# Optimization experiments

Measured on AMD Instinct MI355X. Metric: run time of the kernel, lower is better.

## Reference

```python
import jax, jax.numpy as jnp
import numpy as np

BN_EPS = 1e-5


def setup_inputs() -> dict:
    key = jax.random.key(0)
    ks = jax.random.split(key, 8)
    B, T, D, Tu, Dout, M = 32, 4096, 128, 512, 64, 8
    feats = jax.random.normal(ks[0], (B, T, D), dtype=jnp.float32)
    # integer time-window ids stored in channel 0 of x; pin 0 and Tu-1 so
    # tw_uniq = arange(0, Tu) exactly (no -99 padding) for every batch row
    tw = jax.random.randint(ks[1], (B, T), 0, Tu)
    tw = tw.at[:, 0].set(0).at[:, 1].set(Tu - 1)
    x = jnp.concatenate([tw[..., None].astype(jnp.float32), feats], axis=-1)
    mask = jax.random.uniform(ks[2], (B, T, 1)) < 0.9
    mask = mask.at[:, :2].set(True)  # keep pinned min/max entries valid
    tw_uniq = jnp.broadcast_to(jnp.arange(Tu, dtype=jnp.float32)[None, :, None], (B, Tu, 1))
    bn_gamma = jax.random.uniform(ks[3], (D,), jnp.float32, 0.5, 1.5)
    bn_beta = 0.1 * jax.random.normal(ks[4], (D,), dtype=jnp.float32)
    bn_mean = jnp.zeros((D,), jnp.float32)
    bn_var = jnp.ones((D,), jnp.float32)
    conv_w = jax.random.normal(ks[5], (Dout, D), dtype=jnp.float32) / np.float32(np.sqrt(D))
    conv_b = jnp.zeros((Dout,), jnp.float32)
    fc_w = jax.random.normal(ks[6], (M, Dout), dtype=jnp.float32) / np.float32(np.sqrt(Dout))
    fc_b = jnp.zeros((M,), jnp.float32)
    return dict(x=x, mask=mask, tw_uniq=tw_uniq, bn_gamma=bn_gamma, bn_beta=bn_beta,
                bn_mean=bn_mean, bn_var=bn_var, conv_w=conv_w, conv_b=conv_b,
                fc_w=fc_w, fc_b=fc_b)


def reference(x, mask, tw_uniq, bn_gamma, bn_beta, bn_mean, bn_var,
              conv_w, conv_b, fc_w, fc_b):
    # --- TimeWindowPooling (segment-max form of the dense expand+where+amax) ---
    # torch computes amax_T(where(tw==tw_uniq & mask, x, 0)) -> max(0, group max).
    # Equivalent: scatter-max of mask-zeroed values into a zeros-initialized
    # (B, Tu, D) buffer, avoiding the O(B*T*Tu*D) blowup.
    tw = x[..., 0]           # (B, T) integer-valued, detached in torch
    feats = x[..., 1:]       # (B, T, D)
    B, T, D = feats.shape
    Tu = tw_uniq.shape[1]
    u0 = tw_uniq[:, 0, 0]    # per-batch window minimum
    idx = jnp.clip((tw - u0[:, None]).astype(jnp.int32), 0, Tu - 1)  # (B, T)
    vals = jnp.where(mask, feats, 0.0)  # masked rows contribute 0 == init value
    hidden = jnp.zeros((B, Tu, D), feats.dtype).at[jnp.arange(B)[:, None], idx].max(vals)
    # --- mlp_down: BatchNorm1d (inference stats) + 1x1 Conv1d over channels ---
    h = (hidden - bn_mean) * jax.lax.rsqrt(bn_var + BN_EPS) * bn_gamma + bn_beta
    h = jnp.einsum('bud,od->buo', h, conv_w) + conv_b  # (B, Tu, Dout)
    # --- fc_out ---
    return jnp.einsum('buo,mo->bum', h, fc_w) + fc_b   # (B, Tu, M)
```

## Files before the change

### kernel.cpp

```cpp
#include <hip/hip_runtime.h>

#define B_   32
#define T_   4096
#define D_   128
#define TU   512
#define M_   8
#define O_   64
#define BN_EPS 1e-5f

typedef float f4u __attribute__((ext_vector_type(4), aligned(4)));

#define WS_UIDX   0
#define WS_BASE   (B_ * T_)
#define WS_END    (WS_BASE + B_ * TU)
#define WS_ROWIDX (WS_END + B_ * TU)


__global__ __launch_bounds__(256) void index_kernel(
    const float* __restrict__ x, const int* __restrict__ mask,
    const float* __restrict__ tw_uniq, int* __restrict__ wsI) {
    const int g = blockIdx.x * 256 + threadIdx.x;
    const int b = g >> 12;
    const float twf = x[(size_t)g * (D_ + 1)];
    const int   mk  = mask[g];
    const float u0  = tw_uniq[b * TU];
    const int   u   = min(max((int)(twf - u0), 0), TU - 1);
    wsI[WS_UIDX + g] = mk ? u : -1;
}

__global__ __launch_bounds__(1024) void build_kernel(int* __restrict__ wsI) {
    __shared__ int cnt[TU];
    __shared__ int scn[TU];
    __shared__ int cur[TU];
    const int b = blockIdx.x;
    const int tid = threadIdx.x;
    if (tid < TU) cnt[tid] = 0;
    __syncthreads();
    const int* ub = wsI + WS_UIDX + b * T_;
    int uv[4];
#pragma unroll
    for (int r = 0; r < 4; ++r) {
        uv[r] = ub[r * 1024 + tid];
        if (uv[r] >= 0) atomicAdd(&cnt[uv[r]], 1);
    }
    __syncthreads();
    if (tid < TU) scn[tid] = cnt[tid];
    __syncthreads();
    for (int off = 1; off < TU; off <<= 1) {
        int v = 0;
        if (tid < TU && tid >= off) v = scn[tid - off];
        __syncthreads();
        if (tid < TU) scn[tid] += v;
        __syncthreads();
    }
    if (tid < TU) {
        const int e = scn[tid];
        const int s = e - cnt[tid];
        wsI[WS_BASE + b * TU + tid] = s;
        wsI[WS_END  + b * TU + tid] = e;
        cur[tid] = s;
    }
    __syncthreads();
    int* rb = wsI + WS_ROWIDX + b * T_;
#pragma unroll
    for (int r = 0; r < 4; ++r) {
        if (uv[r] >= 0) {
            const int pos = atomicAdd(&cur[uv[r]], 1);
            rb[pos] = r * 1024 + tid;
        }
    }
}

__global__ __launch_bounds__(1024) void gather_mm_kernel(
    const float* __restrict__ x,
    const float* __restrict__ bn_gamma, const float* __restrict__ bn_beta,
    const float* __restrict__ bn_mean,  const float* __restrict__ bn_var,
    const float* __restrict__ conv_w,   const float* __restrict__ conv_b,
    const float* __restrict__ fc_w,     const float* __restrict__ fc_b,
    const int* __restrict__ wsI, float* __restrict__ out) {
    __shared__ float wsm[M_ * D_];
    __shared__ float tmp[M_ * D_];
    __shared__ float biasc[M_];
    const int j = blockIdx.x;
    const int b  = (j & 7) + 8 * ((j >> 3) & 3);
    const int uc = j >> 5;
    const int tid = threadIdx.x;

    {
        const int m = tid >> 7, d = tid & (D_ - 1);
        float wraw = 0.f;
        for (int o = 0; o < O_; ++o) wraw += fc_w[m * O_ + o] * conv_w[o * D_ + d];
        const float sc = bn_gamma[d] * rsqrtf(bn_var[d] + BN_EPS);
        const float sh = bn_beta[d] - bn_mean[d] * sc;
        wsm[tid] = wraw * sc;
        tmp[tid] = wraw * sh;
    }
    __syncthreads();
    if (tid < M_) {
        float s = fc_b[tid];
        for (int o = 0; o < O_; ++o) s += fc_w[tid * O_ + o] * conv_b[o];
        for (int d = 0; d < D_; ++d) s += tmp[tid * D_ + d];
        biasc[tid] = s;
    }
    __syncthreads();

    const int w    = tid >> 6;
    const int lane = tid & 63;
    const int half = lane >> 5;
    const int lq   = lane & 31;
    const float* xb = x + (size_t)b * T_ * (D_ + 1);
    const int* rowb = wsI + WS_ROWIDX + b * T_;

    for (int k = 0; k < 4; ++k) {
        const int u = uc * 64 + w * 4 + k;
        const int start = wsI[WS_BASE + b * TU + u];
        const int end   = wsI[WS_END  + b * TU + u];
        float a0 = 0.f, a1 = 0.f, a2 = 0.f, a3 = 0.f;
        int  r    = start + half;
        bool have = r < end;
        f4u  vn;
        if (have) { vn = *(const f4u*)(xb + (size_t)rowb[r] * (D_ + 1) + 1 + lq * 4); r += 2; }
        while (have) {
            const f4u v = vn;
            have = r < end;
            if (have) { vn = *(const f4u*)(xb + (size_t)rowb[r] * (D_ + 1) + 1 + lq * 4); r += 2; }
            a0 = fmaxf(a0, v.x); a1 = fmaxf(a1, v.y);
            a2 = fmaxf(a2, v.z); a3 = fmaxf(a3, v.w);
        }
        a0 = fmaxf(a0, __shfl_xor(a0, 32)); a1 = fmaxf(a1, __shfl_xor(a1, 32));
        a2 = fmaxf(a2, __shfl_xor(a2, 32)); a3 = fmaxf(a3, __shfl_xor(a3, 32));

        const int db = lq * 4;
        float p0, p1, p2, p3, p4, p5, p6, p7;
#define PDOT(mm) (a0 * wsm[(mm) * D_ + db] + a1 * wsm[(mm) * D_ + db + 1] + \
                  a2 * wsm[(mm) * D_ + db + 2] + a3 * wsm[(mm) * D_ + db + 3])
        p0 = PDOT(0); p1 = PDOT(1); p2 = PDOT(2); p3 = PDOT(3);
        p4 = PDOT(4); p5 = PDOT(5); p6 = PDOT(6); p7 = PDOT(7);
#undef PDOT
#pragma unroll
        for (int off = 1; off < 32; off <<= 1) {
            p0 += __shfl_xor(p0, off); p1 += __shfl_xor(p1, off);
            p2 += __shfl_xor(p2, off); p3 += __shfl_xor(p3, off);
            p4 += __shfl_xor(p4, off); p5 += __shfl_xor(p5, off);
            p6 += __shfl_xor(p6, off); p7 += __shfl_xor(p7, off);
        }
        if (lane == 0) {
            float* op = out + ((size_t)(b * TU + u)) * M_;
            *(float4*)(op)     = make_float4(p0 + biasc[0], p1 + biasc[1],
                                             p2 + biasc[2], p3 + biasc[3]);
            *(float4*)(op + 4) = make_float4(p4 + biasc[4], p5 + biasc[5],
                                             p6 + biasc[6], p7 + biasc[7]);
        }
    }
}

extern "C" void kernel_launch(void* const* d_in, const int* in_sizes, int n_in,
                              void* d_out, int out_size, void* d_ws, size_t ws_size,
                              hipStream_t stream) {
    const float* x        = (const float*)d_in[0];
    const int*   mask     = (const int*)  d_in[1];
    const float* tw_uniq  = (const float*)d_in[2];
    const float* bn_gamma = (const float*)d_in[3];
    const float* bn_beta  = (const float*)d_in[4];
    const float* bn_mean  = (const float*)d_in[5];
    const float* bn_var   = (const float*)d_in[6];
    const float* conv_w   = (const float*)d_in[7];
    const float* conv_b   = (const float*)d_in[8];
    const float* fc_w     = (const float*)d_in[9];
    const float* fc_b     = (const float*)d_in[10];
    int*   wsI = (int*)d_ws;
    float* out = (float*)d_out;

    index_kernel<<<512, 256, 0, stream>>>(x, mask, tw_uniq, wsI);
    build_kernel<<<32, 1024, 0, stream>>>(wsI);
    gather_mm_kernel<<<256, 1024, 0, stream>>>(
        x, bn_gamma, bn_beta, bn_mean, bn_var,
        conv_w, conv_b, fc_w, fc_b, wsI, out);
}
```

Before: 141.6 us.

## Fuse index pass into build kernel and give each half-wave its own window

The separate index kernel is folded into the per-batch build kernel, which computes window ids straight from x and mask and keeps them in shared memory. The gather kernel now assigns one window per half-wavefront rather than four windows per wavefront. It doubles the grid and batches up to 8 row loads at a time, using row indices broadcast by shuffle, to raise memory-level parallelism. This removes one launch and a global round trip, but only 32 blocks now read the strided x timestamps, and the extra gather blocks repeat the weight-folding prologue.

```diff
diff --git a/kernel.cpp b/kernel.cpp
--- a/kernel.cpp
+++ b/kernel.cpp
@@ -10,25 +10,15 @@
 
 typedef float f4u __attribute__((ext_vector_type(4), aligned(4)));
 
-#define WS_UIDX   0
-#define WS_BASE   (B_ * T_)
-#define WS_END    (WS_BASE + B_ * TU)
-#define WS_ROWIDX (WS_END + B_ * TU)
+#define WS_BASE   0
+#define WS_END    (B_ * TU)
+#define WS_ROWIDX (2 * B_ * TU)
 
 
-__global__ __launch_bounds__(256) void index_kernel(
+__global__ __launch_bounds__(1024) void build_kernel(
     const float* __restrict__ x, const int* __restrict__ mask,
     const float* __restrict__ tw_uniq, int* __restrict__ wsI) {
-    const int g = blockIdx.x * 256 + threadIdx.x;
-    const int b = g >> 12;
-    const float twf = x[(size_t)g * (D_ + 1)];
-    const int   mk  = mask[g];
-    const float u0  = tw_uniq[b * TU];
-    const int   u   = min(max((int)(twf - u0), 0), TU - 1);
-    wsI[WS_UIDX + g] = mk ? u : -1;
-}
-
-__global__ __launch_bounds__(1024) void build_kernel(int* __restrict__ wsI) {
+    __shared__ int uloc[T_];
     __shared__ int cnt[TU];
     __shared__ int scn[TU];
     __shared__ int cur[TU];
@@ -36,12 +26,17 @@
     const int tid = threadIdx.x;
     if (tid < TU) cnt[tid] = 0;
     __syncthreads();
-    const int* ub = wsI + WS_UIDX + b * T_;
-    int uv[4];
+    const float* xb = x + (size_t)b * T_ * (D_ + 1);
+    const int*   mb = mask + b * T_;
+    const float  u0 = tw_uniq[b * TU];
 #pragma unroll
     for (int r = 0; r < 4; ++r) {
-        uv[r] = ub[r * 1024 + tid];
-        if (uv[r] >= 0) atomicAdd(&cnt[uv[r]], 1);
+        const int t = r * 1024 + tid;
+        const float twf = xb[(size_t)t * (D_ + 1)];
+        const int   mk  = mb[t];
+        const int   u   = min(max((int)(twf - u0), 0), TU - 1);
+        uloc[t] = mk ? u : -1;
+        if (mk) atomicAdd(&cnt[u], 1);
     }
     __syncthreads();
     if (tid < TU) scn[tid] = cnt[tid];
@@ -64,14 +59,16 @@
     int* rb = wsI + WS_ROWIDX + b * T_;
 #pragma unroll
     for (int r = 0; r < 4; ++r) {
-        if (uv[r] >= 0) {
-            const int pos = atomicAdd(&cur[uv[r]], 1);
-            rb[pos] = r * 1024 + tid;
+        const int t = r * 1024 + tid;
+        const int u = uloc[t];
+        if (u >= 0) {
+            const int pos = atomicAdd(&cur[u], 1);
+            rb[pos] = t;
         }
     }
 }
 
-__global__ __launch_bounds__(1024) void gather_mm_kernel(
+__global__ __launch_bounds__(1024, 4) void gather_mm_kernel(
     const float* __restrict__ x,
     const float* __restrict__ bn_gamma, const float* __restrict__ bn_beta,
     const float* __restrict__ bn_mean,  const float* __restrict__ bn_var,
@@ -111,46 +108,63 @@
     const float* xb = x + (size_t)b * T_ * (D_ + 1);
     const int* rowb = wsI + WS_ROWIDX + b * T_;
 
-    for (int k = 0; k < 4; ++k) {
-        const int u = uc * 64 + w * 4 + k;
-        const int start = wsI[WS_BASE + b * TU + u];
-        const int end   = wsI[WS_END  + b * TU + u];
-        float a0 = 0.f, a1 = 0.f, a2 = 0.f, a3 = 0.f;
-        int  r    = start + half;
-        bool have = r < end;
-        f4u  vn;
-        if (have) { vn = *(const f4u*)(xb + (size_t)rowb[r] * (D_ + 1) + 1 + lq * 4); r += 2; }
-        while (have) {
-            const f4u v = vn;
-            have = r < end;
-            if (have) { vn = *(const f4u*)(xb + (size_t)rowb[r] * (D_ + 1) + 1 + lq * 4); r += 2; }
-            a0 = fmaxf(a0, v.x); a1 = fmaxf(a1, v.y);
-            a2 = fmaxf(a2, v.z); a3 = fmaxf(a3, v.w);
-        }
-        a0 = fmaxf(a0, __shfl_xor(a0, 32)); a1 = fmaxf(a1, __shfl_xor(a1, 32));
-        a2 = fmaxf(a2, __shfl_xor(a2, 32)); a3 = fmaxf(a3, __shfl_xor(a3, 32));
+    const int u     = uc * 32 + w * 2 + half;
+    const int start = wsI[WS_BASE + b * TU + u];
+    const int end   = wsI[WS_END  + b * TU + u];
+    const int n     = end - start;
+    const int nn    = min(n, 32);
+    int myidx = 0;
+    if (lq < n) myidx = rowb[start + lq];
 
-        const int db = lq * 4;
-        float p0, p1, p2, p3, p4, p5, p6, p7;
+    float a0 = 0.f, a1 = 0.f, a2 = 0.f, a3 = 0.f;
+#define ROWP(i) (const f4u*)(xb + (size_t)__shfl(myidx, (half << 5) + (i)) * (D_ + 1) + 1 + (lq << 2))
+    for (int bs = 0; bs < nn; bs += 8) {
+        const int m = nn - bs;
+        f4u t0, t1, t2, t3, t4, t5, t6, t7;
+        if (m > 0) t0 = *ROWP(bs + 0);
+        if (m > 1) t1 = *ROWP(bs + 1);
+        if (m > 2) t2 = *ROWP(bs + 2);
+        if (m > 3) t3 = *ROWP(bs + 3);
+        if (m > 4) t4 = *ROWP(bs + 4);
+        if (m > 5) t5 = *ROWP(bs + 5);
+        if (m > 6) t6 = *ROWP(bs + 6);
+        if (m > 7) t7 = *ROWP(bs + 7);
+        if (m > 0) { a0 = fmaxf(a0, t0.x); a1 = fmaxf(a1, t0.y); a2 = fmaxf(a2, t0.z); a3 = fmaxf(a3, t0.w); }
+        if (m > 1) { a0 = fmaxf(a0, t1.x); a1 = fmaxf(a1, t1.y); a2 = fmaxf(a2, t1.z); a3 = fmaxf(a3, t1.w); }
+        if (m > 2) { a0 = fmaxf(a0, t2.x); a1 = fmaxf(a1, t2.y); a2 = fmaxf(a2, t2.z); a3 = fmaxf(a3, t2.w); }
+        if (m > 3) { a0 = fmaxf(a0, t3.x); a1 = fmaxf(a1, t3.y); a2 = fmaxf(a2, t3.z); a3 = fmaxf(a3, t3.w); }
+        if (m > 4) { a0 = fmaxf(a0, t4.x); a1 = fmaxf(a1, t4.y); a2 = fmaxf(a2, t4.z); a3 = fmaxf(a3, t4.w); }
+        if (m > 5) { a0 = fmaxf(a0, t5.x); a1 = fmaxf(a1, t5.y); a2 = fmaxf(a2, t5.z); a3 = fmaxf(a3, t5.w); }
+        if (m > 6) { a0 = fmaxf(a0, t6.x); a1 = fmaxf(a1, t6.y); a2 = fmaxf(a2, t6.z); a3 = fmaxf(a3, t6.w); }
+        if (m > 7) { a0 = fmaxf(a0, t7.x); a1 = fmaxf(a1, t7.y); a2 = fmaxf(a2, t7.z); a3 = fmaxf(a3, t7.w); }
+    }
+#undef ROWP
+    for (int r = start + 32; r < end; ++r) {
+        const f4u v = *(const f4u*)(xb + (size_t)rowb[r] * (D_ + 1) + 1 + (lq << 2));
+        a0 = fmaxf(a0, v.x); a1 = fmaxf(a1, v.y);
+        a2 = fmaxf(a2, v.z); a3 = fmaxf(a3, v.w);
+    }
+
+    const int db = lq << 2;
+    float p0, p1, p2, p3, p4, p5, p6, p7;
 #define PDOT(mm) (a0 * wsm[(mm) * D_ + db] + a1 * wsm[(mm) * D_ + db + 1] + \
                   a2 * wsm[(mm) * D_ + db + 2] + a3 * wsm[(mm) * D_ + db + 3])
-        p0 = PDOT(0); p1 = PDOT(1); p2 = PDOT(2); p3 = PDOT(3);
-        p4 = PDOT(4); p5 = PDOT(5); p6 = PDOT(6); p7 = PDOT(7);
+    p0 = PDOT(0); p1 = PDOT(1); p2 = PDOT(2); p3 = PDOT(3);
+    p4 = PDOT(4); p5 = PDOT(5); p6 = PDOT(6); p7 = PDOT(7);
 #undef PDOT
 #pragma unroll
-        for (int off = 1; off < 32; off <<= 1) {
-            p0 += __shfl_xor(p0, off); p1 += __shfl_xor(p1, off);
-            p2 += __shfl_xor(p2, off); p3 += __shfl_xor(p3, off);
-            p4 += __shfl_xor(p4, off); p5 += __shfl_xor(p5, off);
-            p6 += __shfl_xor(p6, off); p7 += __shfl_xor(p7, off);
-        }
-        if (lane == 0) {
-            float* op = out + ((size_t)(b * TU + u)) * M_;
-            *(float4*)(op)     = make_float4(p0 + biasc[0], p1 + biasc[1],
-                                             p2 + biasc[2], p3 + biasc[3]);
-            *(float4*)(op + 4) = make_float4(p4 + biasc[4], p5 + biasc[5],
-                                             p6 + biasc[6], p7 + biasc[7]);
-        }
+    for (int off = 1; off < 32; off <<= 1) {
+        p0 += __shfl_xor(p0, off); p1 += __shfl_xor(p1, off);
+        p2 += __shfl_xor(p2, off); p3 += __shfl_xor(p3, off);
+        p4 += __shfl_xor(p4, off); p5 += __shfl_xor(p5, off);
+        p6 += __shfl_xor(p6, off); p7 += __shfl_xor(p7, off);
+    }
+    if (lq == 0) {
+        float* op = out + ((size_t)(b * TU + u)) * M_;
+        *(float4*)(op)     = make_float4(p0 + biasc[0], p1 + biasc[1],
+                                         p2 + biasc[2], p3 + biasc[3]);
+        *(float4*)(op + 4) = make_float4(p4 + biasc[4], p5 + biasc[5],
+                                         p6 + biasc[6], p7 + biasc[7]);
     }
 }
 
@@ -171,9 +185,8 @@
     int*   wsI = (int*)d_ws;
     float* out = (float*)d_out;
 
-    index_kernel<<<512, 256, 0, stream>>>(x, mask, tw_uniq, wsI);
-    build_kernel<<<32, 1024, 0, stream>>>(wsI);
-    gather_mm_kernel<<<256, 1024, 0, stream>>>(
+    build_kernel<<<32, 1024, 0, stream>>>(x, mask, tw_uniq, wsI);
+    gather_mm_kernel<<<512, 1024, 0, stream>>>(
         x, bn_gamma, bn_beta, bn_mean, bn_var,
         conv_w, conv_b, fc_w, fc_b, wsI, out);
 }
```

After: 137.0 us. 3.3% less time.
